# Performance work log

Measured on AMD Instinct MI355X. Metric: run time of the kernel, lower is better.

The kernel has to match this reference:

```python
import jax, jax.numpy as jnp
import numpy as np
import math

N, E, D, H, L, DIN, NEP = 20000, 320000, 128, 8, 4, 16, 4
DFF = 4 * D
DH = D // H
SCALE = 1.0 / math.sqrt(DH)


def _ln(x, s, b, eps=1e-5):
    mu = x.mean(-1, keepdims=True)
    var = ((x - mu) ** 2).mean(-1, keepdims=True)
    return (x - mu) * jax.lax.rsqrt(var + eps) * s + b


def _attn(h, src, dst, ew, Wq, Wk, Wv, Wo, Wo_b):
    n = h.shape[0]
    Q = (h @ Wq).reshape(n, H, DH)
    K = (h @ Wk).reshape(n, H, DH)
    V = (h @ Wv).reshape(n, H, DH)
    # per-edge scores: [E, H]; ew is sigmoid(edge_feat.sum(-1, keepdims)) -> [E, 1]
    scores = (Q[src] * K[dst]).sum(-1) * SCALE * ew
    msg = V[dst] * scores[:, :, None]                       # [E, H, DH]
    sums = jax.ops.segment_sum(msg, dst, num_segments=n)    # [N, H, DH]
    cnt = jax.ops.segment_sum(jnp.ones((msg.shape[0],), h.dtype), dst, num_segments=n)
    out = sums / jnp.maximum(cnt, 1.0)[:, None, None]       # segment-mean (zeros if no edges)
    return out.reshape(n, D) @ Wo + Wo_b


def setup_inputs() -> dict:
    key = jax.random.key(0)
    ks = iter(jax.random.split(key, 40))
    rn = lambda *s: jax.random.normal(next(ks), s, jnp.float32) * 0.02
    inp = {
        'x': jax.random.normal(next(ks), (N, DIN), jnp.float32),
        'edge_index': jax.random.randint(next(ks), (2, E), 0, N),
        'edge_attr': jax.random.normal(next(ks), (E, 1), jnp.float32),
        'in_w': rn(DIN, D), 'in_b': jnp.zeros((D,)),
        'ee_w1': rn(1, D // 4), 'ee_b1': jnp.zeros((D // 4,)),
        'ee_w2': rn(D // 4, D // 2), 'ee_b2': jnp.zeros((D // 2,)),
        'Wq': rn(L, D, D), 'Wk': rn(L, D, D), 'Wv': rn(L, D, D),
        'Wo': rn(L, D, D), 'Wo_b': jnp.zeros((L, D)),
        'ff_w1': rn(L, D, DFF), 'ff_b1': jnp.zeros((L, DFF)),
        'ff_w2': rn(L, DFF, D), 'ff_b2': jnp.zeros((L, D)),
        'ln1_s': jnp.ones((L, D)), 'ln1_b': jnp.zeros((L, D)),
        'ln2_s': jnp.ones((L, D)), 'ln2_b': jnp.zeros((L, D)),
        'ec_w1': rn(D * 2 + D // 2, D), 'ec_b1': jnp.zeros((D,)),
        'ec_w2': rn(D, D // 2), 'ec_b2': jnp.zeros((D // 2,)),
        'ec_w3': rn(D // 2, 1), 'ec_b3': jnp.zeros((1,)),
        'pp_w1': rn(D * 2 + D // 2, D), 'pp_b1': jnp.zeros((D,)),
        'pp_w2': rn(D, D // 2), 'pp_b2': jnp.zeros((D // 2,)),
        'pp_w3': rn(D // 2, NEP), 'pp_b3': jnp.zeros((NEP,)),
    }
    return inp


def reference(x, edge_index, edge_attr, in_w, in_b, ee_w1, ee_b1, ee_w2, ee_b2,
              Wq, Wk, Wv, Wo, Wo_b, ff_w1, ff_b1, ff_w2, ff_b2,
              ln1_s, ln1_b, ln2_s, ln2_b,
              ec_w1, ec_b1, ec_w2, ec_b2, ec_w3, ec_b3,
              pp_w1, pp_b1, pp_w2, pp_b2, pp_w3, pp_b3):
    src, dst = edge_index[0], edge_index[1]
    h = x @ in_w + in_b                                     # [N, D]
    edge_feat = jax.nn.relu(edge_attr @ ee_w1 + ee_b1) @ ee_w2 + ee_b2  # [E, D/2]
    ew = jax.nn.sigmoid(edge_feat.sum(-1, keepdims=True))   # [E, 1]
    for l in range(L):
        a = _attn(h, src, dst, ew, Wq[l], Wk[l], Wv[l], Wo[l], Wo_b[l])
        h = _ln(h + a, ln1_s[l], ln1_b[l])
        f = jax.nn.relu(h @ ff_w1[l] + ff_b1[l]) @ ff_w2[l] + ff_b2[l]
        h = _ln(h + f, ln2_s[l], ln2_b[l])
    ef = jnp.concatenate([h[src], h[dst], edge_feat], axis=1)  # [E, 2.5*D]
    z = jax.nn.relu(ef @ ec_w1 + ec_b1)
    z = jax.nn.relu(z @ ec_w2 + ec_b2)
    edge_logits = (z @ ec_w3 + ec_b3).squeeze(-1)
    p = jax.nn.relu(ef @ pp_w1 + pp_b1)
    p = jax.nn.relu(p @ pp_w2 + pp_b2)
    edge_params = jax.nn.softplus(p @ pp_w3 + pp_b3) + 1e-6
    return edge_logits, edge_params
```

## Files before the change

kernel.cpp:

```cpp
#include <hip/hip_runtime.h>
#include <hip/hip_bf16.h>
#include <math.h>

#define N_NODES 20000
#define N_EDGES 320000
#define D 128
#define DFF 512
#define DIN 16
#define NLAYER 4
#define SCALE 0.25f
#define KE1 288

typedef __hip_bfloat16 bf16;
typedef __attribute__((ext_vector_type(8))) __bf16 bf16x8_t;
typedef __attribute__((ext_vector_type(4))) float f32x4;

__global__ void k_input_proj(const float* __restrict__ x, const float* __restrict__ in_w,
                             const float* __restrict__ in_b, float* __restrict__ h,
                             __bf16* __restrict__ h_bf) {
  int node = blockIdx.x;
  int j = threadIdx.x;
  __shared__ float xs[DIN];
  if (j < DIN) xs[j] = x[node * DIN + j];
  __syncthreads();
  float acc = in_b[j];
  for (int k = 0; k < DIN; ++k) acc = fmaf(xs[k], in_w[k * D + j], acc);
  h[(size_t)node * D + j] = acc;
  h_bf[(size_t)node * D + j] = (__bf16)acc;
}

__global__ void k_edge_prep(const float* __restrict__ ea, const float* __restrict__ w1,
                            const float* __restrict__ b1, const float* __restrict__ w2,
                            const float* __restrict__ b2, const int* __restrict__ dst,
                            float* __restrict__ ew, float* __restrict__ cnt) {
  __shared__ float rs[32], w1s[32], b1s[32];
  __shared__ float b2sum;
  int tid = threadIdx.x;
  if (tid < 32) {
    float s = 0.f;
    for (int j = 0; j < 64; ++j) s += w2[tid * 64 + j];
    rs[tid] = s;
    w1s[tid] = w1[tid];
    b1s[tid] = b1[tid];
  }
  if (tid == 0) {
    float s = 0.f;
    for (int j = 0; j < 64; ++j) s += b2[j];
    b2sum = s;
  }
  __syncthreads();
  int e = blockIdx.x * blockDim.x + tid;
  if (e >= N_EDGES) return;
  float a = ea[e];
  float s = b2sum;
  for (int i = 0; i < 32; ++i) {
    float t = fmaxf(fmaf(a, w1s[i], b1s[i]), 0.f);
    s = fmaf(t, rs[i], s);
  }
  ew[e] = 1.f / (1.f + expf(-s));
  atomicAdd(&cnt[dst[e]], 1.f);
}

__global__ void k_cvt_all(const float* __restrict__ Wq, const float* __restrict__ Wk,
                          const float* __restrict__ Wv, const float* __restrict__ ffw1,
                          const float* __restrict__ ffw2, const float* __restrict__ Wo,
                          const float* __restrict__ ecw2, const float* __restrict__ ppw2,
                          __bf16* __restrict__ wqkvT, __bf16* __restrict__ w1T,
                          __bf16* __restrict__ w2T, __bf16* __restrict__ woT,
                          __bf16* __restrict__ w2ET, __bf16* __restrict__ w2PT) {
  int t = blockIdx.x * 256 + threadIdx.x;
  if (t < 196608) {
    int l = t / 49152, u = t % 49152;
    int m = u / 16384, v = u % 16384;
    int n = v / 128, k = v % 128;
    const float* W = (m == 0) ? Wq : (m == 1) ? Wk : Wv;
    wqkvT[t] = (__bf16)W[l * 16384 + k * 128 + n];
  } else if (t < 196608 + 262144) {
    int u = t - 196608;
    int l = u / 65536, v = u % 65536;
    int n = v / 128, k = v % 128;
    w1T[u] = (__bf16)ffw1[l * 65536 + k * 512 + n];
  } else if (t < 458752 + 262144) {
    int u = t - 458752;
    int l = u / 65536, v = u % 65536;
    int n = v / 512, k = v % 512;
    w2T[u] = (__bf16)ffw2[l * 65536 + k * 128 + n];
  } else if (t < 720896 + 65536) {
    int u = t - 720896;
    int l = u / 16384, v = u % 16384;
    int n = v / 128, k = v % 128;
    woT[u] = (__bf16)Wo[l * 16384 + k * 128 + n];
  } else if (t < 786432 + 8192) {
    int u = t - 786432;
    int n = u / 128, k = u % 128;
    w2ET[u] = (__bf16)ecw2[k * 64 + n];
  } else if (t < 794624 + 8192) {
    int u = t - 794624;
    int n = u / 128, k = u % 128;
    w2PT[u] = (__bf16)ppw2[k * 64 + n];
  }
}

__global__ void k_prep(const float* __restrict__ ec_w1, const float* __restrict__ ec_b1,
                       const float* __restrict__ pp_w1, const float* __restrict__ pp_b1,
                       const float* __restrict__ ee_w2, const float* __restrict__ ee_b2,
                       __bf16* __restrict__ w1ET, __bf16* __restrict__ w1PT,
                       float* __restrict__ b1Ep, float* __restrict__ b1Pp) {
  int tid = threadIdx.x;
  int p = tid >> 7, n = tid & 127;
  const float* w1 = p ? pp_w1 : ec_w1;
  const float* bb = p ? pp_b1 : ec_b1;
  __bf16* wT = p ? w1PT : w1ET;
  float* bo = p ? b1Pp : b1Ep;
  for (int k = 0; k < 256; ++k) wT[n * KE1 + k] = (__bf16)w1[k * 128 + n];
  for (int i = 0; i < 32; ++i) {
    float m = 0.f;
    for (int j = 0; j < 64; ++j) m = fmaf(ee_w2[i * 64 + j], w1[(256 + j) * 128 + n], m);
    wT[n * KE1 + 256 + i] = (__bf16)m;
  }
  float b = bb[n];
  for (int j = 0; j < 64; ++j) b = fmaf(ee_b2[j], w1[(256 + j) * 128 + n], b);
  bo[n] = b;
}

__global__ __launch_bounds__(256) void k_qkv(const __bf16* __restrict__ h_bf,
                                             const __bf16* __restrict__ wT,
                                             __bf16* __restrict__ Q, __bf16* __restrict__ K,
                                             __bf16* __restrict__ V) {
  int tid = threadIdx.x, wv = tid >> 6, lane = tid & 63;
  int lr = lane & 15, lk = (lane >> 4) * 8, g4 = (lane >> 4) * 4;
  int n0 = blockIdx.x * 16;
  const __bf16* hp = h_bf + (size_t)(n0 + lr) * D;
  f32x4 acc[6];
#pragma unroll
  for (int j = 0; j < 6; ++j) acc[j] = (f32x4){0.f, 0.f, 0.f, 0.f};
#pragma unroll
  for (int ks = 0; ks < 4; ++ks) {
    bf16x8_t aF = *(const bf16x8_t*)&hp[ks * 32 + lk];
#pragma unroll
    for (int j = 0; j < 6; ++j) {
      int nb = wv * 6 + j;
      bf16x8_t bF = *(const bf16x8_t*)&wT[(nb * 16 + lr) * 128 + ks * 32 + lk];
      acc[j] = __builtin_amdgcn_mfma_f32_16x16x32_bf16(aF, bF, acc[j], 0, 0, 0);
    }
  }
#pragma unroll
  for (int j = 0; j < 6; ++j) {
    int nb = wv * 6 + j;
    int m = nb >> 3;
    __bf16* out = (m == 0) ? Q : (m == 1) ? K : V;
#pragma unroll
    for (int r = 0; r < 4; ++r)
      out[(size_t)(n0 + g4 + r) * D + (nb & 7) * 16 + lr] = (__bf16)acc[j][r];
  }
}

__global__ void k_edge_attn(const int* __restrict__ src, const int* __restrict__ dst,
                            const float* __restrict__ ew, const __bf16* __restrict__ Q,
                            const __bf16* __restrict__ K, float* __restrict__ sc) {
  int t = blockIdx.x * blockDim.x + threadIdx.x;
  if (t >= N_EDGES * 8) return;
  int e = t >> 3, hd = t & 7;
  int s = src[e], d = dst[e];
  const __bf16* q = Q + (size_t)s * D + hd * 16;
  const __bf16* k = K + (size_t)d * D + hd * 16;
  bf16x8_t q0 = *(const bf16x8_t*)q, q1 = *(const bf16x8_t*)(q + 8);
  bf16x8_t k0 = *(const bf16x8_t*)k, k1 = *(const bf16x8_t*)(k + 8);
  float p = 0.f;
#pragma unroll
  for (int i = 0; i < 8; ++i) p = fmaf((float)q0[i], (float)k0[i], p);
#pragma unroll
  for (int i = 0; i < 8; ++i) p = fmaf((float)q1[i], (float)k1[i], p);
  atomicAdd(&sc[d * 8 + hd], p * SCALE * ew[e]);
}

__global__ __launch_bounds__(256) void k_node(
    float* __restrict__ sc, const float* __restrict__ cnt, const __bf16* __restrict__ Vin,
    float* __restrict__ h, __bf16* __restrict__ h_bf, const __bf16* __restrict__ woT,
    const float* __restrict__ Wo_b, const float* __restrict__ ln1_s,
    const float* __restrict__ ln1_b, const __bf16* __restrict__ w1T,
    const __bf16* __restrict__ w2T, const float* __restrict__ b1,
    const float* __restrict__ b2, const float* __restrict__ ln2_s,
    const float* __restrict__ ln2_b, const __bf16* __restrict__ wqkvT_next,
    __bf16* __restrict__ Q, __bf16* __restrict__ K, __bf16* __restrict__ Vout) {
  __shared__ __bf16 z0[16][136];
  __shared__ __bf16 z1[16][520];
  __shared__ float lnb[4][16][2];
  int tid = threadIdx.x, wv = tid >> 6, lane = tid & 63;
  int lr = lane & 15, lk = (lane >> 4) * 8, g4 = (lane >> 4) * 4;
  int n0 = blockIdx.x * 16;
  int nd = n0 + lr;

  float inv = 1.f / fmaxf(cnt[nd], 1.f);
  float scs[8];
#pragma unroll
  for (int i = 0; i < 8; ++i) scs[i] = sc[nd * 8 + i] * inv;
  f32x4 acc[2];
#pragma unroll
  for (int j = 0; j < 2; ++j) {
    float bv = Wo_b[(wv * 2 + j) * 16 + lr];
    acc[j] = (f32x4){bv, bv, bv, bv};
  }
#pragma unroll
  for (int ks = 0; ks < 4; ++ks) {
    bf16x8_t v8 = *(const bf16x8_t*)&Vin[(size_t)nd * D + ks * 32 + lk];
    float m = scs[(ks * 32 + lk) >> 4];
    bf16x8_t aF;
#pragma unroll
    for (int i = 0; i < 8; ++i) aF[i] = (__bf16)((float)v8[i] * m);
#pragma unroll
    for (int j = 0; j < 2; ++j) {
      bf16x8_t bF = *(const bf16x8_t*)&woT[((wv * 2 + j) * 16 + lr) * 128 + ks * 32 + lk];
      acc[j] = __builtin_amdgcn_mfma_f32_16x16x32_bf16(aF, bF, acc[j], 0, 0, 0);
    }
  }
  float y[2][4];
#pragma unroll
  for (int j = 0; j < 2; ++j)
#pragma unroll
    for (int r = 0; r < 4; ++r)
      y[j][r] = h[(size_t)(n0 + g4 + r) * D + (wv * 2 + j) * 16 + lr] + acc[j][r];
  float s_[4], q_[4];
#pragma unroll
  for (int r = 0; r < 4; ++r) {
    float a0 = y[0][r], a1 = y[1][r];
    float s = a0 + a1, q = fmaf(a0, a0, a1 * a1);
    s += __shfl_xor(s, 1); s += __shfl_xor(s, 2); s += __shfl_xor(s, 4); s += __shfl_xor(s, 8);
    q += __shfl_xor(q, 1); q += __shfl_xor(q, 2); q += __shfl_xor(q, 4); q += __shfl_xor(q, 8);
    s_[r] = s; q_[r] = q;
  }
  if (lr == 0) {
#pragma unroll
    for (int r = 0; r < 4; ++r) {
      lnb[wv][g4 + r][0] = s_[r];
      lnb[wv][g4 + r][1] = q_[r];
    }
  }
  __syncthreads();
  if (tid < 128) sc[n0 * 8 + tid] = 0.f;
  float mean[4], rstd[4];
#pragma unroll
  for (int r = 0; r < 4; ++r) {
    float sm = 0.f, sq = 0.f;
#pragma unroll
    for (int w2i = 0; w2i < 4; ++w2i) {
      sm += lnb[w2i][g4 + r][0];
      sq += lnb[w2i][g4 + r][1];
    }
    float mu = sm * (1.f / 128.f);
    mean[r] = mu;
    rstd[r] = rsqrtf(sq * (1.f / 128.f) - mu * mu + 1e-5f);
  }
#pragma unroll
  for (int j = 0; j < 2; ++j) {
    int col = (wv * 2 + j) * 16 + lr;
    float lsv = ln1_s[col], lbv = ln1_b[col];
#pragma unroll
    for (int r = 0; r < 4; ++r) {
      y[j][r] = (y[j][r] - mean[r]) * rstd[r] * lsv + lbv;
      z0[g4 + r][col] = (__bf16)y[j][r];
    }
  }
  __syncthreads();

  f32x4 a1[8];
#pragma unroll
  for (int j = 0; j < 8; ++j) {
    float bv = b1[(wv * 8 + j) * 16 + lr];
    a1[j] = (f32x4){bv, bv, bv, bv};
  }
#pragma unroll
  for (int ks = 0; ks < 4; ++ks) {
    bf16x8_t aF = *(const bf16x8_t*)&z0[lr][ks * 32 + lk];
#pragma unroll
    for (int j = 0; j < 8; ++j) {
      bf16x8_t bF = *(const bf16x8_t*)&w1T[((wv * 8 + j) * 16 + lr) * 128 + ks * 32 + lk];
      a1[j] = __builtin_amdgcn_mfma_f32_16x16x32_bf16(aF, bF, a1[j], 0, 0, 0);
    }
  }
#pragma unroll
  for (int j = 0; j < 8; ++j)
#pragma unroll
    for (int r = 0; r < 4; ++r)
      z1[g4 + r][(wv * 8 + j) * 16 + lr] = (__bf16)fmaxf(a1[j][r], 0.f);
  __syncthreads();

  f32x4 a2[2];
#pragma unroll
  for (int j = 0; j < 2; ++j) {
    float bv = b2[(wv * 2 + j) * 16 + lr];
    a2[j] = (f32x4){bv, bv, bv, bv};
  }
#pragma unroll
  for (int ks = 0; ks < 16; ++ks) {
    bf16x8_t aF = *(const bf16x8_t*)&z1[lr][ks * 32 + lk];
#pragma unroll
    for (int j = 0; j < 2; ++j) {
      bf16x8_t bF = *(const bf16x8_t*)&w2T[((wv * 2 + j) * 16 + lr) * 512 + ks * 32 + lk];
      a2[j] = __builtin_amdgcn_mfma_f32_16x16x32_bf16(aF, bF, a2[j], 0, 0, 0);
    }
  }
#pragma unroll
  for (int j = 0; j < 2; ++j)
#pragma unroll
    for (int r = 0; r < 4; ++r) y[j][r] += a2[j][r];
#pragma unroll
  for (int r = 0; r < 4; ++r) {
    float a0 = y[0][r], a1v = y[1][r];
    float s = a0 + a1v, q = fmaf(a0, a0, a1v * a1v);
    s += __shfl_xor(s, 1); s += __shfl_xor(s, 2); s += __shfl_xor(s, 4); s += __shfl_xor(s, 8);
    q += __shfl_xor(q, 1); q += __shfl_xor(q, 2); q += __shfl_xor(q, 4); q += __shfl_xor(q, 8);
    s_[r] = s; q_[r] = q;
  }
  if (lr == 0) {
#pragma unroll
    for (int r = 0; r < 4; ++r) {
      lnb[wv][g4 + r][0] = s_[r];
      lnb[wv][g4 + r][1] = q_[r];
    }
  }
  __syncthreads();
#pragma unroll
  for (int r = 0; r < 4; ++r) {
    float sm = 0.f, sq = 0.f;
#pragma unroll
    for (int w2i = 0; w2i < 4; ++w2i) {
      sm += lnb[w2i][g4 + r][0];
      sq += lnb[w2i][g4 + r][1];
    }
    float mu = sm * (1.f / 128.f);
    mean[r] = mu;
    rstd[r] = rsqrtf(sq * (1.f / 128.f) - mu * mu + 1e-5f);
  }
#pragma unroll
  for (int j = 0; j < 2; ++j) {
    int col = (wv * 2 + j) * 16 + lr;
    float lsv = ln2_s[col], lbv = ln2_b[col];
#pragma unroll
    for (int r = 0; r < 4; ++r) {
      float yv = (y[j][r] - mean[r]) * rstd[r] * lsv + lbv;
      y[j][r] = yv;
      h[(size_t)(n0 + g4 + r) * D + col] = yv;
      h_bf[(size_t)(n0 + g4 + r) * D + col] = (__bf16)yv;
    }
  }

  if (wqkvT_next) {
#pragma unroll
    for (int j = 0; j < 2; ++j)
#pragma unroll
      for (int r = 0; r < 4; ++r)
        z0[g4 + r][(wv * 2 + j) * 16 + lr] = (__bf16)y[j][r];
    __syncthreads();
    f32x4 aq[6];
#pragma unroll
    for (int j = 0; j < 6; ++j) aq[j] = (f32x4){0.f, 0.f, 0.f, 0.f};
#pragma unroll
    for (int ks = 0; ks < 4; ++ks) {
      bf16x8_t aF = *(const bf16x8_t*)&z0[lr][ks * 32 + lk];
#pragma unroll
      for (int j = 0; j < 6; ++j) {
        int nb = wv * 6 + j;
        bf16x8_t bF = *(const bf16x8_t*)&wqkvT_next[(nb * 16 + lr) * 128 + ks * 32 + lk];
        aq[j] = __builtin_amdgcn_mfma_f32_16x16x32_bf16(aF, bF, aq[j], 0, 0, 0);
      }
    }
#pragma unroll
    for (int j = 0; j < 6; ++j) {
      int nb = wv * 6 + j;
      int m = nb >> 3;
      __bf16* out = (m == 0) ? Q : (m == 1) ? K : Vout;
#pragma unroll
      for (int r = 0; r < 4; ++r)
        out[(size_t)(n0 + g4 + r) * D + (nb & 7) * 16 + lr] = (__bf16)aq[j][r];
    }
  }
}

__global__ __launch_bounds__(256) void k_pnode(const __bf16* __restrict__ h_bf,
                                               const __bf16* __restrict__ w1ET,
                                               const __bf16* __restrict__ w1PT,
                                               __bf16* __restrict__ PsE,
                                               __bf16* __restrict__ PdE,
                                               __bf16* __restrict__ PsP,
                                               __bf16* __restrict__ PdP) {
  int tid = threadIdx.x, wv = tid >> 6, lane = tid & 63;
  int lr = lane & 15, lk = (lane >> 4) * 8, g4 = (lane >> 4) * 4;
  int n0 = blockIdx.x * 16;
  const __bf16* hp = h_bf + (size_t)(n0 + lr) * D;
  const __bf16* wsrc = (wv & 2) ? w1PT : w1ET;
  int koff = (wv & 1) ? 128 : 0;
  __bf16* out = (wv == 0) ? PsE : (wv == 1) ? PdE : (wv == 2) ? PsP : PdP;
  f32x4 acc[8];
#pragma unroll
  for (int nb = 0; nb < 8; ++nb) acc[nb] = (f32x4){0.f, 0.f, 0.f, 0.f};
#pragma unroll
  for (int ks = 0; ks < 4; ++ks) {
    bf16x8_t aF = *(const bf16x8_t*)&hp[ks * 32 + lk];
#pragma unroll
    for (int nb = 0; nb < 8; ++nb) {
      bf16x8_t bF = *(const bf16x8_t*)&wsrc[(nb * 16 + lr) * KE1 + koff + ks * 32 + lk];
      acc[nb] = __builtin_amdgcn_mfma_f32_16x16x32_bf16(aF, bF, acc[nb], 0, 0, 0);
    }
  }
#pragma unroll
  for (int nb = 0; nb < 8; ++nb)
#pragma unroll
    for (int r = 0; r < 4; ++r)
      out[(size_t)(n0 + g4 + r) * D + nb * 16 + lr] = (__bf16)acc[nb][r];
}

__global__ __launch_bounds__(256) void k_final(
    const int* __restrict__ src, const int* __restrict__ dst, const float* __restrict__ ea,
    const float* __restrict__ ee_w1, const float* __restrict__ ee_b1,
    const __bf16* __restrict__ w1ET, const __bf16* __restrict__ w1PT,
    const __bf16* __restrict__ w2ET, const __bf16* __restrict__ w2PT,
    const float* __restrict__ b1Ep, const float* __restrict__ b1Pp,
    const __bf16* __restrict__ PsE, const __bf16* __restrict__ PdE,
    const __bf16* __restrict__ PsP, const __bf16* __restrict__ PdP,
    const float* __restrict__ ec_b2, const float* __restrict__ ec_w3,
    const float* __restrict__ ec_b3, const float* __restrict__ pp_b2,
    const float* __restrict__ pp_w3, const float* __restrict__ pp_b3,
    float* __restrict__ out_logits, float* __restrict__ out_params) {
  __shared__ __bf16 z1[2][32][136];
  __shared__ __bf16 zf[4][16][136];
  int tid = threadIdx.x, wv = tid >> 6, lane = tid & 63;
  int lr = lane & 15, lk = (lane >> 4) * 8, g4 = (lane >> 4) * 4;
  int p = wv & 1, m0 = (wv >> 1) * 16;
  int e0 = blockIdx.x * 32;
  int e = e0 + m0 + lr;
  float av = ea[e];
  bf16x8_t aR;
#pragma unroll
  for (int i = 0; i < 8; ++i)
    aR[i] = (__bf16)fmaxf(fmaf(av, ee_w1[lk + i], ee_b1[lk + i]), 0.f);

  const __bf16* w1x = p ? w1PT : w1ET;
  const float* b1x = p ? b1Pp : b1Ep;
  const __bf16* w2x = p ? w2PT : w2ET;
  const float* b2x = p ? pp_b2 : ec_b2;

  f32x4 acc[8];
#pragma unroll
  for (int nb = 0; nb < 8; ++nb) {
    float bv = b1x[nb * 16 + lr];
    acc[nb] = (f32x4){bv, bv, bv, bv};
  }
#pragma unroll
  for (int nb = 0; nb < 8; ++nb) {
    bf16x8_t bF = *(const bf16x8_t*)&w1x[(nb * 16 + lr) * KE1 + 256 + lk];
    acc[nb] = __builtin_amdgcn_mfma_f32_16x16x32_bf16(aR, bF, acc[nb], 0, 0, 0);
  }
#pragma unroll
  for (int nb = 0; nb < 8; ++nb)
#pragma unroll
    for (int r = 0; r < 4; ++r) zf[wv][g4 + r][nb * 16 + lr] = (__bf16)acc[nb][r];

  {
    int em = lane >> 2, c4 = lane & 3;
    int ee = e0 + m0 + em;
    const __bf16* Ps = p ? PsP : PsE;
    const __bf16* Pd = p ? PdP : PdE;
    const __bf16* psrow = Ps + (size_t)src[ee] * D + c4 * 32;
    const __bf16* pdrow = Pd + (size_t)dst[ee] * D + c4 * 32;
#pragma unroll
    for (int ch = 0; ch < 4; ++ch) {
      bf16x8_t a = *(const bf16x8_t*)&psrow[ch * 8];
      bf16x8_t b = *(const bf16x8_t*)&pdrow[ch * 8];
      bf16x8_t f = *(const bf16x8_t*)&zf[wv][em][c4 * 32 + ch * 8];
      bf16x8_t o;
#pragma unroll
      for (int i = 0; i < 8; ++i)
        o[i] = (__bf16)fmaxf((float)a[i] + (float)b[i] + (float)f[i], 0.f);
      *(bf16x8_t*)&z1[p][m0 + em][c4 * 32 + ch * 8] = o;
    }
  }

  f32x4 acc2[4];
#pragma unroll
  for (int nb = 0; nb < 4; ++nb) {
    float bv = b2x[nb * 16 + lr];
    acc2[nb] = (f32x4){bv, bv, bv, bv};
  }
#pragma unroll
  for (int ks = 0; ks < 4; ++ks) {
    bf16x8_t aF = *(const bf16x8_t*)&z1[p][m0 + lr][ks * 32 + lk];
#pragma unroll
    for (int nb = 0; nb < 4; ++nb) {
      bf16x8_t bF = *(const bf16x8_t*)&w2x[(nb * 16 + lr) * 128 + ks * 32 + lk];
      acc2[nb] = __builtin_amdgcn_mfma_f32_16x16x32_bf16(aF, bF, acc2[nb], 0, 0, 0);
    }
  }

  if (p == 0) {
    float w3v[4];
#pragma unroll
    for (int nb = 0; nb < 4; ++nb) w3v[nb] = ec_w3[nb * 16 + lr];
    float b3 = ec_b3[0];
#pragma unroll
    for (int r = 0; r < 4; ++r) {
      float s = 0.f;
#pragma unroll
      for (int nb = 0; nb < 4; ++nb) s = fmaf(fmaxf(acc2[nb][r], 0.f), w3v[nb], s);
      s += __shfl_xor(s, 1);
      s += __shfl_xor(s, 2);
      s += __shfl_xor(s, 4);
      s += __shfl_xor(s, 8);
      if (lr == 0) out_logits[e0 + m0 + g4 + r] = s + b3;
    }
  } else {
    float wp[4][4];
#pragma unroll
    for (int nb = 0; nb < 4; ++nb)
#pragma unroll
      for (int c = 0; c < 4; ++c) wp[nb][c] = pp_w3[(nb * 16 + lr) * 4 + c];
#pragma unroll
    for (int c = 0; c < 4; ++c) {
      float b3 = pp_b3[c];
#pragma unroll
      for (int r = 0; r < 4; ++r) {
        float s = 0.f;
#pragma unroll
        for (int nb = 0; nb < 4; ++nb) s = fmaf(fmaxf(acc2[nb][r], 0.f), wp[nb][c], s);
        s += __shfl_xor(s, 1);
        s += __shfl_xor(s, 2);
        s += __shfl_xor(s, 4);
        s += __shfl_xor(s, 8);
        if (lr == 0) {
          float xx = s + b3;
          float sp = fmaxf(xx, 0.f) + log1pf(expf(-fabsf(xx)));
          out_params[(size_t)(e0 + m0 + g4 + r) * 4 + c] = sp + 1e-6f;
        }
      }
    }
  }
}

extern "C" void kernel_launch(void* const* d_in, const int* in_sizes, int n_in,
                              void* d_out, int out_size, void* d_ws, size_t ws_size,
                              hipStream_t stream) {
  const float* x = (const float*)d_in[0];
  const int* eidx = (const int*)d_in[1];
  const float* eattr = (const float*)d_in[2];
  const float* in_w = (const float*)d_in[3];
  const float* in_b = (const float*)d_in[4];
  const float* ee_w1 = (const float*)d_in[5];
  const float* ee_b1 = (const float*)d_in[6];
  const float* ee_w2 = (const float*)d_in[7];
  const float* ee_b2 = (const float*)d_in[8];
  const float* Wq = (const float*)d_in[9];
  const float* Wk = (const float*)d_in[10];
  const float* Wv = (const float*)d_in[11];
  const float* Wo = (const float*)d_in[12];
  const float* Wo_b = (const float*)d_in[13];
  const float* ff_w1 = (const float*)d_in[14];
  const float* ff_b1 = (const float*)d_in[15];
  const float* ff_w2 = (const float*)d_in[16];
  const float* ff_b2 = (const float*)d_in[17];
  const float* ln1_s = (const float*)d_in[18];
  const float* ln1_b = (const float*)d_in[19];
  const float* ln2_s = (const float*)d_in[20];
  const float* ln2_b = (const float*)d_in[21];
  const float* ec_w1 = (const float*)d_in[22];
  const float* ec_b1 = (const float*)d_in[23];
  const float* ec_w2 = (const float*)d_in[24];
  const float* ec_b2 = (const float*)d_in[25];
  const float* ec_w3 = (const float*)d_in[26];
  const float* ec_b3 = (const float*)d_in[27];
  const float* pp_w1 = (const float*)d_in[28];
  const float* pp_b1 = (const float*)d_in[29];
  const float* pp_w2 = (const float*)d_in[30];
  const float* pp_b2 = (const float*)d_in[31];
  const float* pp_w3 = (const float*)d_in[32];
  const float* pp_b3 = (const float*)d_in[33];

  const int* src = eidx;
  const int* dst = eidx + N_EDGES;

  char* wsb = (char*)d_ws;
  float* sc = (float*)wsb;
  float* cnt = (float*)(wsb + 640000);
  float* h = (float*)(wsb + 720000);
  __bf16* h_bf = (__bf16*)(wsb + 10960000);
  __bf16* Q = (__bf16*)(wsb + 16080000);
  __bf16* Kb = (__bf16*)(wsb + 21200000);
  __bf16* V0 = (__bf16*)(wsb + 26320000);
  __bf16* V1 = (__bf16*)(wsb + 31440000);
  float* ew = (float*)(wsb + 36560000);
  __bf16* wqkvT = (__bf16*)(wsb + 37840000);
  __bf16* w1T = (__bf16*)(wsb + 38233216);
  __bf16* w2T = (__bf16*)(wsb + 38757504);
  __bf16* woT = (__bf16*)(wsb + 39281792);
  __bf16* w1ET = (__bf16*)(wsb + 39412864);
  __bf16* w1PT = (__bf16*)(wsb + 39486592);
  __bf16* w2ET = (__bf16*)(wsb + 39560320);
  __bf16* w2PT = (__bf16*)(wsb + 39576704);
  float* b1Ep = (float*)(wsb + 39593088);
  float* b1Pp = (float*)(wsb + 39593600);

  hipMemsetAsync(cnt, 0, N_NODES * sizeof(float), stream);
  hipMemsetAsync(sc, 0, N_NODES * 8 * sizeof(float), stream);
  k_input_proj<<<N_NODES, D, 0, stream>>>(x, in_w, in_b, h, h_bf);
  k_edge_prep<<<(N_EDGES + 255) / 256, 256, 0, stream>>>(eattr, ee_w1, ee_b1, ee_w2, ee_b2,
                                                         dst, ew, cnt);
  k_cvt_all<<<(802816 + 255) / 256, 256, 0, stream>>>(Wq, Wk, Wv, ff_w1, ff_w2, Wo, ec_w2,
                                                      pp_w2, wqkvT, w1T, w2T, woT, w2ET, w2PT);
  k_prep<<<1, 256, 0, stream>>>(ec_w1, ec_b1, pp_w1, pp_b1, ee_w2, ee_b2, w1ET, w1PT, b1Ep,
                                b1Pp);

  int nblk = N_NODES / 16;
  k_qkv<<<nblk, 256, 0, stream>>>(h_bf, wqkvT, Q, Kb, V0);
  for (int l = 0; l < NLAYER; ++l) {
    __bf16* Vin = (l & 1) ? V1 : V0;
    __bf16* Vout = (l & 1) ? V0 : V1;
    k_edge_attn<<<(N_EDGES * 8 + 255) / 256, 256, 0, stream>>>(src, dst, ew, Q, Kb, sc);
    k_node<<<nblk, 256, 0, stream>>>(
        sc, cnt, Vin, h, h_bf, woT + (size_t)l * 16384, Wo_b + l * D, ln1_s + l * D,
        ln1_b + l * D, w1T + (size_t)l * 65536, w2T + (size_t)l * 65536, ff_b1 + l * DFF,
        ff_b2 + l * D, ln2_s + l * D, ln2_b + l * D,
        (l < NLAYER - 1) ? (wqkvT + (size_t)(l + 1) * 49152) : (const __bf16*)nullptr, Q, Kb,
        Vout);
  }

  __bf16* PsE = Q;
  __bf16* PdE = Kb;
  __bf16* PsP = V0;
  __bf16* PdP = V1;
  k_pnode<<<nblk, 256, 0, stream>>>(h_bf, w1ET, w1PT, PsE, PdE, PsP, PdP);

  float* out_logits = (float*)d_out;
  float* out_params = out_logits + N_EDGES;
  k_final<<<N_EDGES / 32, 256, 0, stream>>>(src, dst, eattr, ee_w1, ee_b1, w1ET, w1PT, w2ET,
                                            w2PT, b1Ep, b1Pp, PsE, PdE, PsP, PdP, ec_b2,
                                            ec_w3, ec_b3, pp_b2, pp_w3, pp_b3, out_logits,
                                            out_params);
}
```

Baseline: 615.3 us.

## Replace atomic edge attention with dst-sorted CSR gather and fuse edge-node projection

Builds a destination-sorted CSR once, using a single-block prefix scan over counts and then an atomic-cursor scatter of src and edge weight. Per-layer attention then runs one wave per destination node. Each wave first accumulates the weighted sum of the gathered Q rows and takes one dot product with K[d], using linearity. This removes the per-edge, per-head float atomics and the per-layer memset of scores. The separate k_pnode projection is folded into the last layer's k_node, which reuses the LayerNorm output already held in shared memory. The cost is a serial one-block scan, an extra scatter pass, and an edge order inside each CSR segment that is not deterministic.

```diff
diff --git a/kernel.cpp b/kernel.cpp
--- a/kernel.cpp
+++ b/kernel.cpp
@@ -13,6 +13,7 @@
 
 typedef __hip_bfloat16 bf16;
 typedef __attribute__((ext_vector_type(8))) __bf16 bf16x8_t;
+typedef __attribute__((ext_vector_type(2))) __bf16 bf16x2_t;
 typedef __attribute__((ext_vector_type(4))) float f32x4;
 
 __global__ void k_input_proj(const float* __restrict__ x, const float* __restrict__ in_w,
@@ -59,6 +60,48 @@
   }
   ew[e] = 1.f / (1.f + expf(-s));
   atomicAdd(&cnt[dst[e]], 1.f);
+}
+
+__global__ __launch_bounds__(1024) void k_scan(const float* __restrict__ cnt,
+                                               int* __restrict__ off,
+                                               int* __restrict__ cursor) {
+  __shared__ int ts[1024];
+  int tid = threadIdx.x;
+  const int per = (N_NODES + 1023) / 1024;
+  int base = tid * per;
+  int s = 0;
+  for (int i = 0; i < per; ++i) {
+    int idx = base + i;
+    if (idx < N_NODES) s += (int)cnt[idx];
+  }
+  ts[tid] = s;
+  __syncthreads();
+  for (int st = 1; st < 1024; st <<= 1) {
+    int v = (tid >= st) ? ts[tid - st] : 0;
+    __syncthreads();
+    ts[tid] += v;
+    __syncthreads();
+  }
+  int run = (tid == 0) ? 0 : ts[tid - 1];
+  for (int i = 0; i < per; ++i) {
+    int idx = base + i;
+    if (idx < N_NODES) {
+      off[idx] = run;
+      cursor[idx] = run;
+      run += (int)cnt[idx];
+    }
+  }
+  if (tid == 1023) off[N_NODES] = run;
+}
+
+__global__ void k_scatter(const int* __restrict__ src, const int* __restrict__ dst,
+                          const float* __restrict__ ew, int* __restrict__ cursor,
+                          int* __restrict__ csr_src, float* __restrict__ csr_ew) {
+  int e = blockIdx.x * blockDim.x + threadIdx.x;
+  if (e >= N_EDGES) return;
+  int pos = atomicAdd(&cursor[dst[e]], 1);
+  csr_src[pos] = src[e];
+  csr_ew[pos] = ew[e];
 }
 
 __global__ void k_cvt_all(const float* __restrict__ Wq, const float* __restrict__ Wk,
@@ -155,34 +198,54 @@
   }
 }
 
-__global__ void k_edge_attn(const int* __restrict__ src, const int* __restrict__ dst,
-                            const float* __restrict__ ew, const __bf16* __restrict__ Q,
-                            const __bf16* __restrict__ K, float* __restrict__ sc) {
-  int t = blockIdx.x * blockDim.x + threadIdx.x;
-  if (t >= N_EDGES * 8) return;
-  int e = t >> 3, hd = t & 7;
-  int s = src[e], d = dst[e];
-  const __bf16* q = Q + (size_t)s * D + hd * 16;
-  const __bf16* k = K + (size_t)d * D + hd * 16;
-  bf16x8_t q0 = *(const bf16x8_t*)q, q1 = *(const bf16x8_t*)(q + 8);
-  bf16x8_t k0 = *(const bf16x8_t*)k, k1 = *(const bf16x8_t*)(k + 8);
-  float p = 0.f;
-#pragma unroll
-  for (int i = 0; i < 8; ++i) p = fmaf((float)q0[i], (float)k0[i], p);
-#pragma unroll
-  for (int i = 0; i < 8; ++i) p = fmaf((float)q1[i], (float)k1[i], p);
-  atomicAdd(&sc[d * 8 + hd], p * SCALE * ew[e]);
+__global__ __launch_bounds__(256) void k_attn_csr(const int* __restrict__ off,
+                                                  const int* __restrict__ csr_src,
+                                                  const float* __restrict__ csr_ew,
+                                                  const __bf16* __restrict__ Q,
+                                                  const __bf16* __restrict__ K,
+                                                  float* __restrict__ sc) {
+  int wv = threadIdx.x >> 6, lane = threadIdx.x & 63;
+  int d = blockIdx.x * 4 + wv;
+  bf16x2_t k2 = *(const bf16x2_t*)(K + (size_t)d * D + lane * 2);
+  float t0 = 0.f, t1 = 0.f;
+  int i = off[d], end = off[d + 1];
+  int s_next = 0;
+  float w_next = 0.f;
+  if (i < end) {
+    s_next = csr_src[i];
+    w_next = csr_ew[i];
+  }
+  while (i < end) {
+    int s = s_next;
+    float w = w_next;
+    ++i;
+    if (i < end) {
+      s_next = csr_src[i];
+      w_next = csr_ew[i];
+    }
+    bf16x2_t q2 = *(const bf16x2_t*)(Q + (size_t)s * D + lane * 2);
+    t0 = fmaf(w, (float)q2[0], t0);
+    t1 = fmaf(w, (float)q2[1], t1);
+  }
+  float p = fmaf(t0, (float)k2[0], t1 * (float)k2[1]);
+  p += __shfl_xor(p, 1);
+  p += __shfl_xor(p, 2);
+  p += __shfl_xor(p, 4);
+  if ((lane & 7) == 0) sc[d * 8 + (lane >> 3)] = p * SCALE;
 }
 
 __global__ __launch_bounds__(256) void k_node(
-    float* __restrict__ sc, const float* __restrict__ cnt, const __bf16* __restrict__ Vin,
-    float* __restrict__ h, __bf16* __restrict__ h_bf, const __bf16* __restrict__ woT,
-    const float* __restrict__ Wo_b, const float* __restrict__ ln1_s,
-    const float* __restrict__ ln1_b, const __bf16* __restrict__ w1T,
-    const __bf16* __restrict__ w2T, const float* __restrict__ b1,
-    const float* __restrict__ b2, const float* __restrict__ ln2_s,
-    const float* __restrict__ ln2_b, const __bf16* __restrict__ wqkvT_next,
-    __bf16* __restrict__ Q, __bf16* __restrict__ K, __bf16* __restrict__ Vout) {
+    const float* __restrict__ sc, const float* __restrict__ cnt,
+    const __bf16* __restrict__ Vin, float* __restrict__ h, __bf16* __restrict__ h_bf,
+    const __bf16* __restrict__ woT, const float* __restrict__ Wo_b,
+    const float* __restrict__ ln1_s, const float* __restrict__ ln1_b,
+    const __bf16* __restrict__ w1T, const __bf16* __restrict__ w2T,
+    const float* __restrict__ b1, const float* __restrict__ b2,
+    const float* __restrict__ ln2_s, const float* __restrict__ ln2_b,
+    const __bf16* __restrict__ wqkvT_next, __bf16* __restrict__ Q, __bf16* __restrict__ K,
+    __bf16* __restrict__ Vout, const __bf16* __restrict__ w1ET,
+    const __bf16* __restrict__ w1PT, __bf16* __restrict__ PsE, __bf16* __restrict__ PdE,
+    __bf16* __restrict__ PsP, __bf16* __restrict__ PdP) {
   __shared__ __bf16 z0[16][136];
   __shared__ __bf16 z1[16][520];
   __shared__ float lnb[4][16][2];
@@ -237,7 +300,6 @@
     }
   }
   __syncthreads();
-  if (tid < 128) sc[n0 * 8 + tid] = 0.f;
   float mean[4], rstd[4];
 #pragma unroll
   for (int r = 0; r < 4; ++r) {
@@ -345,13 +407,14 @@
     }
   }
 
+#pragma unroll
+  for (int j = 0; j < 2; ++j)
+#pragma unroll
+    for (int r = 0; r < 4; ++r)
+      z0[g4 + r][(wv * 2 + j) * 16 + lr] = (__bf16)y[j][r];
+  __syncthreads();
+
   if (wqkvT_next) {
-#pragma unroll
-    for (int j = 0; j < 2; ++j)
-#pragma unroll
-      for (int r = 0; r < 4; ++r)
-        z0[g4 + r][(wv * 2 + j) * 16 + lr] = (__bf16)y[j][r];
-    __syncthreads();
     f32x4 aq[6];
 #pragma unroll
     for (int j = 0; j < 6; ++j) aq[j] = (f32x4){0.f, 0.f, 0.f, 0.f};
@@ -374,40 +437,28 @@
       for (int r = 0; r < 4; ++r)
         out[(size_t)(n0 + g4 + r) * D + (nb & 7) * 16 + lr] = (__bf16)aq[j][r];
     }
-  }
-}
-
-__global__ __launch_bounds__(256) void k_pnode(const __bf16* __restrict__ h_bf,
-                                               const __bf16* __restrict__ w1ET,
-                                               const __bf16* __restrict__ w1PT,
-                                               __bf16* __restrict__ PsE,
-                                               __bf16* __restrict__ PdE,
-                                               __bf16* __restrict__ PsP,
-                                               __bf16* __restrict__ PdP) {
-  int tid = threadIdx.x, wv = tid >> 6, lane = tid & 63;
-  int lr = lane & 15, lk = (lane >> 4) * 8, g4 = (lane >> 4) * 4;
-  int n0 = blockIdx.x * 16;
-  const __bf16* hp = h_bf + (size_t)(n0 + lr) * D;
-  const __bf16* wsrc = (wv & 2) ? w1PT : w1ET;
-  int koff = (wv & 1) ? 128 : 0;
-  __bf16* out = (wv == 0) ? PsE : (wv == 1) ? PdE : (wv == 2) ? PsP : PdP;
-  f32x4 acc[8];
-#pragma unroll
-  for (int nb = 0; nb < 8; ++nb) acc[nb] = (f32x4){0.f, 0.f, 0.f, 0.f};
-#pragma unroll
-  for (int ks = 0; ks < 4; ++ks) {
-    bf16x8_t aF = *(const bf16x8_t*)&hp[ks * 32 + lk];
-#pragma unroll
-    for (int nb = 0; nb < 8; ++nb) {
-      bf16x8_t bF = *(const bf16x8_t*)&wsrc[(nb * 16 + lr) * KE1 + koff + ks * 32 + lk];
-      acc[nb] = __builtin_amdgcn_mfma_f32_16x16x32_bf16(aF, bF, acc[nb], 0, 0, 0);
-    }
-  }
-#pragma unroll
-  for (int nb = 0; nb < 8; ++nb)
-#pragma unroll
-    for (int r = 0; r < 4; ++r)
-      out[(size_t)(n0 + g4 + r) * D + nb * 16 + lr] = (__bf16)acc[nb][r];
+  } else {
+    const __bf16* wsrc = (wv & 2) ? w1PT : w1ET;
+    int koff = (wv & 1) ? 128 : 0;
+    __bf16* outP = (wv == 0) ? PsE : (wv == 1) ? PdE : (wv == 2) ? PsP : PdP;
+    f32x4 ap[8];
+#pragma unroll
+    for (int nb = 0; nb < 8; ++nb) ap[nb] = (f32x4){0.f, 0.f, 0.f, 0.f};
+#pragma unroll
+    for (int ks = 0; ks < 4; ++ks) {
+      bf16x8_t aF = *(const bf16x8_t*)&z0[lr][ks * 32 + lk];
+#pragma unroll
+      for (int nb = 0; nb < 8; ++nb) {
+        bf16x8_t bF = *(const bf16x8_t*)&wsrc[(nb * 16 + lr) * KE1 + koff + ks * 32 + lk];
+        ap[nb] = __builtin_amdgcn_mfma_f32_16x16x32_bf16(aF, bF, ap[nb], 0, 0, 0);
+      }
+    }
+#pragma unroll
+    for (int nb = 0; nb < 8; ++nb)
+#pragma unroll
+      for (int r = 0; r < 4; ++r)
+        outP[(size_t)(n0 + g4 + r) * D + nb * 16 + lr] = (__bf16)ap[nb][r];
+  }
 }
 
 __global__ __launch_bounds__(256) void k_final(
@@ -597,36 +648,40 @@
   __bf16* w2PT = (__bf16*)(wsb + 39576704);
   float* b1Ep = (float*)(wsb + 39593088);
   float* b1Pp = (float*)(wsb + 39593600);
+  int* off = (int*)(wsb + 39594112);
+  int* cursor = (int*)(wsb + 39674128);
+  int* csr_src = (int*)(wsb + 39754128);
+  float* csr_ew = (float*)(wsb + 41034128);
 
   hipMemsetAsync(cnt, 0, N_NODES * sizeof(float), stream);
-  hipMemsetAsync(sc, 0, N_NODES * 8 * sizeof(float), stream);
   k_input_proj<<<N_NODES, D, 0, stream>>>(x, in_w, in_b, h, h_bf);
   k_edge_prep<<<(N_EDGES + 255) / 256, 256, 0, stream>>>(eattr, ee_w1, ee_b1, ee_w2, ee_b2,
                                                          dst, ew, cnt);
+  k_scan<<<1, 1024, 0, stream>>>(cnt, off, cursor);
+  k_scatter<<<(N_EDGES + 255) / 256, 256, 0, stream>>>(src, dst, ew, cursor, csr_src, csr_ew);
   k_cvt_all<<<(802816 + 255) / 256, 256, 0, stream>>>(Wq, Wk, Wv, ff_w1, ff_w2, Wo, ec_w2,
                                                       pp_w2, wqkvT, w1T, w2T, woT, w2ET, w2PT);
   k_prep<<<1, 256, 0, stream>>>(ec_w1, ec_b1, pp_w1, pp_b1, ee_w2, ee_b2, w1ET, w1PT, b1Ep,
                                 b1Pp);
+
+  __bf16* PsE = Q;
+  __bf16* PdE = Kb;
+  __bf16* PsP = V0;
+  __bf16* PdP = V1;
 
   int nblk = N_NODES / 16;
   k_qkv<<<nblk, 256, 0, stream>>>(h_bf, wqkvT, Q, Kb, V0);
   for (int l = 0; l < NLAYER; ++l) {
     __bf16* Vin = (l & 1) ? V1 : V0;
     __bf16* Vout = (l & 1) ? V0 : V1;
-    k_edge_attn<<<(N_EDGES * 8 + 255) / 256, 256, 0, stream>>>(src, dst, ew, Q, Kb, sc);
+    k_attn_csr<<<N_NODES / 4, 256, 0, stream>>>(off, csr_src, csr_ew, Q, Kb, sc);
     k_node<<<nblk, 256, 0, stream>>>(
         sc, cnt, Vin, h, h_bf, woT + (size_t)l * 16384, Wo_b + l * D, ln1_s + l * D,
         ln1_b + l * D, w1T + (size_t)l * 65536, w2T + (size_t)l * 65536, ff_b1 + l * DFF,
         ff_b2 + l * D, ln2_s + l * D, ln2_b + l * D,
         (l < NLAYER - 1) ? (wqkvT + (size_t)(l + 1) * 49152) : (const __bf16*)nullptr, Q, Kb,
-        Vout);
-  }
-
-  __bf16* PsE = Q;
-  __bf16* PdE = Kb;
-  __bf16* PsP = V0;
-  __bf16* PdP = V1;
-  k_pnode<<<nblk, 256, 0, stream>>>(h_bf, w1ET, w1PT, PsE, PdE, PsP, PdP);
+        Vout, w1ET, w1PT, PsE, PdE, PsP, PdP);
+  }
 
   float* out_logits = (float*)d_out;
   float* out_params = out_logits + N_EDGES;
```

Result: slower. 678.0 us (+10.2%).

## Sort edges by destination for final edge MLP and fuse pnode projection into last layer

Applied to the files above, without the earlier changes.

Builds a destination-sorted edge order (counting-sort scan plus atomic scatter) and has the final edge kernel walk edges in that order, gathering PdE/PdP rows with locality and scattering outputs back by original edge id. It also folds the separate per-node edge-head projection kernel into the last k_node launch, reusing the LN output already staged in shared memory. This removes one launch and one re-read of h_bf, and improves cache reuse on dst gathers. It adds a single-block scan, an atomic scatter pass and indirect output writes.

```diff
diff --git a/kernel.cpp b/kernel.cpp
--- a/kernel.cpp
+++ b/kernel.cpp
@@ -59,6 +59,50 @@
   }
   ew[e] = 1.f / (1.f + expf(-s));
   atomicAdd(&cnt[dst[e]], 1.f);
+}
+
+__global__ __launch_bounds__(1024) void k_scan(const float* __restrict__ cnt,
+                                               int* __restrict__ off,
+                                               int* __restrict__ cursor) {
+  __shared__ int ts[1024];
+  int tid = threadIdx.x;
+  const int per = (N_NODES + 1023) / 1024;
+  int base = tid * per;
+  int s = 0;
+  for (int i = 0; i < per; ++i) {
+    int idx = base + i;
+    if (idx < N_NODES) s += (int)cnt[idx];
+  }
+  ts[tid] = s;
+  __syncthreads();
+  for (int st = 1; st < 1024; st <<= 1) {
+    int v = (tid >= st) ? ts[tid - st] : 0;
+    __syncthreads();
+    ts[tid] += v;
+    __syncthreads();
+  }
+  int run = (tid == 0) ? 0 : ts[tid - 1];
+  for (int i = 0; i < per; ++i) {
+    int idx = base + i;
+    if (idx < N_NODES) {
+      off[idx] = run;
+      cursor[idx] = run;
+      run += (int)cnt[idx];
+    }
+  }
+  if (tid == 1023) off[N_NODES] = run;
+}
+
+__global__ void k_scatter(const int* __restrict__ src, const int* __restrict__ dst,
+                          int* __restrict__ cursor, int* __restrict__ csr_src,
+                          int* __restrict__ csr_dst, int* __restrict__ csr_eid) {
+  int e = blockIdx.x * blockDim.x + threadIdx.x;
+  if (e >= N_EDGES) return;
+  int d = dst[e];
+  int pos = atomicAdd(&cursor[d], 1);
+  csr_src[pos] = src[e];
+  csr_dst[pos] = d;
+  csr_eid[pos] = e;
 }
 
 __global__ void k_cvt_all(const float* __restrict__ Wq, const float* __restrict__ Wk,
@@ -182,7 +226,10 @@
     const __bf16* __restrict__ w2T, const float* __restrict__ b1,
     const float* __restrict__ b2, const float* __restrict__ ln2_s,
     const float* __restrict__ ln2_b, const __bf16* __restrict__ wqkvT_next,
-    __bf16* __restrict__ Q, __bf16* __restrict__ K, __bf16* __restrict__ Vout) {
+    __bf16* __restrict__ Q, __bf16* __restrict__ K, __bf16* __restrict__ Vout,
+    const __bf16* __restrict__ w1ET, const __bf16* __restrict__ w1PT,
+    __bf16* __restrict__ PsE, __bf16* __restrict__ PdE, __bf16* __restrict__ PsP,
+    __bf16* __restrict__ PdP) {
   __shared__ __bf16 z0[16][136];
   __shared__ __bf16 z1[16][520];
   __shared__ float lnb[4][16][2];
@@ -345,13 +392,14 @@
     }
   }
 
+#pragma unroll
+  for (int j = 0; j < 2; ++j)
+#pragma unroll
+    for (int r = 0; r < 4; ++r)
+      z0[g4 + r][(wv * 2 + j) * 16 + lr] = (__bf16)y[j][r];
+  __syncthreads();
+
   if (wqkvT_next) {
-#pragma unroll
-    for (int j = 0; j < 2; ++j)
-#pragma unroll
-      for (int r = 0; r < 4; ++r)
-        z0[g4 + r][(wv * 2 + j) * 16 + lr] = (__bf16)y[j][r];
-    __syncthreads();
     f32x4 aq[6];
 #pragma unroll
     for (int j = 0; j < 6; ++j) aq[j] = (f32x4){0.f, 0.f, 0.f, 0.f};
@@ -374,44 +422,33 @@
       for (int r = 0; r < 4; ++r)
         out[(size_t)(n0 + g4 + r) * D + (nb & 7) * 16 + lr] = (__bf16)aq[j][r];
     }
-  }
-}
-
-__global__ __launch_bounds__(256) void k_pnode(const __bf16* __restrict__ h_bf,
-                                               const __bf16* __restrict__ w1ET,
-                                               const __bf16* __restrict__ w1PT,
-                                               __bf16* __restrict__ PsE,
-                                               __bf16* __restrict__ PdE,
-                                               __bf16* __restrict__ PsP,
-                                               __bf16* __restrict__ PdP) {
-  int tid = threadIdx.x, wv = tid >> 6, lane = tid & 63;
-  int lr = lane & 15, lk = (lane >> 4) * 8, g4 = (lane >> 4) * 4;
-  int n0 = blockIdx.x * 16;
-  const __bf16* hp = h_bf + (size_t)(n0 + lr) * D;
-  const __bf16* wsrc = (wv & 2) ? w1PT : w1ET;
-  int koff = (wv & 1) ? 128 : 0;
-  __bf16* out = (wv == 0) ? PsE : (wv == 1) ? PdE : (wv == 2) ? PsP : PdP;
-  f32x4 acc[8];
-#pragma unroll
-  for (int nb = 0; nb < 8; ++nb) acc[nb] = (f32x4){0.f, 0.f, 0.f, 0.f};
-#pragma unroll
-  for (int ks = 0; ks < 4; ++ks) {
-    bf16x8_t aF = *(const bf16x8_t*)&hp[ks * 32 + lk];
-#pragma unroll
-    for (int nb = 0; nb < 8; ++nb) {
-      bf16x8_t bF = *(const bf16x8_t*)&wsrc[(nb * 16 + lr) * KE1 + koff + ks * 32 + lk];
-      acc[nb] = __builtin_amdgcn_mfma_f32_16x16x32_bf16(aF, bF, acc[nb], 0, 0, 0);
-    }
-  }
-#pragma unroll
-  for (int nb = 0; nb < 8; ++nb)
-#pragma unroll
-    for (int r = 0; r < 4; ++r)
-      out[(size_t)(n0 + g4 + r) * D + nb * 16 + lr] = (__bf16)acc[nb][r];
+  } else {
+    const __bf16* wsrc = (wv & 2) ? w1PT : w1ET;
+    int koff = (wv & 1) ? 128 : 0;
+    __bf16* outP = (wv == 0) ? PsE : (wv == 1) ? PdE : (wv == 2) ? PsP : PdP;
+    f32x4 ap[8];
+#pragma unroll
+    for (int nb = 0; nb < 8; ++nb) ap[nb] = (f32x4){0.f, 0.f, 0.f, 0.f};
+#pragma unroll
+    for (int ks = 0; ks < 4; ++ks) {
+      bf16x8_t aF = *(const bf16x8_t*)&z0[lr][ks * 32 + lk];
+#pragma unroll
+      for (int nb = 0; nb < 8; ++nb) {
+        bf16x8_t bF = *(const bf16x8_t*)&wsrc[(nb * 16 + lr) * KE1 + koff + ks * 32 + lk];
+        ap[nb] = __builtin_amdgcn_mfma_f32_16x16x32_bf16(aF, bF, ap[nb], 0, 0, 0);
+      }
+    }
+#pragma unroll
+    for (int nb = 0; nb < 8; ++nb)
+#pragma unroll
+      for (int r = 0; r < 4; ++r)
+        outP[(size_t)(n0 + g4 + r) * D + nb * 16 + lr] = (__bf16)ap[nb][r];
+  }
 }
 
 __global__ __launch_bounds__(256) void k_final(
-    const int* __restrict__ src, const int* __restrict__ dst, const float* __restrict__ ea,
+    const int* __restrict__ csr_src, const int* __restrict__ csr_dst,
+    const int* __restrict__ csr_eid, const float* __restrict__ ea,
     const float* __restrict__ ee_w1, const float* __restrict__ ee_b1,
     const __bf16* __restrict__ w1ET, const __bf16* __restrict__ w1PT,
     const __bf16* __restrict__ w2ET, const __bf16* __restrict__ w2PT,
@@ -429,7 +466,8 @@
   int p = wv & 1, m0 = (wv >> 1) * 16;
   int e0 = blockIdx.x * 32;
   int e = e0 + m0 + lr;
-  float av = ea[e];
+  int eid = csr_eid[e];
+  float av = ea[eid];
   bf16x8_t aR;
 #pragma unroll
   for (int i = 0; i < 8; ++i)
@@ -461,8 +499,8 @@
     int ee = e0 + m0 + em;
     const __bf16* Ps = p ? PsP : PsE;
     const __bf16* Pd = p ? PdP : PdE;
-    const __bf16* psrow = Ps + (size_t)src[ee] * D + c4 * 32;
-    const __bf16* pdrow = Pd + (size_t)dst[ee] * D + c4 * 32;
+    const __bf16* psrow = Ps + (size_t)csr_src[ee] * D + c4 * 32;
+    const __bf16* pdrow = Pd + (size_t)csr_dst[ee] * D + c4 * 32;
 #pragma unroll
     for (int ch = 0; ch < 4; ++ch) {
       bf16x8_t a = *(const bf16x8_t*)&psrow[ch * 8];
@@ -506,7 +544,7 @@
       s += __shfl_xor(s, 2);
       s += __shfl_xor(s, 4);
       s += __shfl_xor(s, 8);
-      if (lr == 0) out_logits[e0 + m0 + g4 + r] = s + b3;
+      if (lr == 0) out_logits[csr_eid[e0 + m0 + g4 + r]] = s + b3;
     }
   } else {
     float wp[4][4];
@@ -529,7 +567,7 @@
         if (lr == 0) {
           float xx = s + b3;
           float sp = fmaxf(xx, 0.f) + log1pf(expf(-fabsf(xx)));
-          out_params[(size_t)(e0 + m0 + g4 + r) * 4 + c] = sp + 1e-6f;
+          out_params[(size_t)csr_eid[e0 + m0 + g4 + r] * 4 + c] = sp + 1e-6f;
         }
       }
     }
@@ -597,16 +635,29 @@
   __bf16* w2PT = (__bf16*)(wsb + 39576704);
   float* b1Ep = (float*)(wsb + 39593088);
   float* b1Pp = (float*)(wsb + 39593600);
+  int* off = (int*)(wsb + 39594112);
+  int* cursor = (int*)(wsb + 39674128);
+  int* csr_src = (int*)(wsb + 39754128);
+  int* csr_dst = (int*)(wsb + 41034128);
+  int* csr_eid = (int*)(wsb + 42314128);
 
   hipMemsetAsync(cnt, 0, N_NODES * sizeof(float), stream);
   hipMemsetAsync(sc, 0, N_NODES * 8 * sizeof(float), stream);
   k_input_proj<<<N_NODES, D, 0, stream>>>(x, in_w, in_b, h, h_bf);
   k_edge_prep<<<(N_EDGES + 255) / 256, 256, 0, stream>>>(eattr, ee_w1, ee_b1, ee_w2, ee_b2,
                                                          dst, ew, cnt);
+  k_scan<<<1, 1024, 0, stream>>>(cnt, off, cursor);
+  k_scatter<<<(N_EDGES + 255) / 256, 256, 0, stream>>>(src, dst, cursor, csr_src, csr_dst,
+                                                       csr_eid);
   k_cvt_all<<<(802816 + 255) / 256, 256, 0, stream>>>(Wq, Wk, Wv, ff_w1, ff_w2, Wo, ec_w2,
                                                       pp_w2, wqkvT, w1T, w2T, woT, w2ET, w2PT);
   k_prep<<<1, 256, 0, stream>>>(ec_w1, ec_b1, pp_w1, pp_b1, ee_w2, ee_b2, w1ET, w1PT, b1Ep,
                                 b1Pp);
+
+  __bf16* PsE = Q;
+  __bf16* PdE = Kb;
+  __bf16* PsP = V0;
+  __bf16* PdP = V1;
 
   int nblk = N_NODES / 16;
   k_qkv<<<nblk, 256, 0, stream>>>(h_bf, wqkvT, Q, Kb, V0);
@@ -619,19 +670,13 @@
         ln1_b + l * D, w1T + (size_t)l * 65536, w2T + (size_t)l * 65536, ff_b1 + l * DFF,
         ff_b2 + l * D, ln2_s + l * D, ln2_b + l * D,
         (l < NLAYER - 1) ? (wqkvT + (size_t)(l + 1) * 49152) : (const __bf16*)nullptr, Q, Kb,
-        Vout);
-  }
-
-  __bf16* PsE = Q;
-  __bf16* PdE = Kb;
-  __bf16* PsP = V0;
-  __bf16* PdP = V1;
-  k_pnode<<<nblk, 256, 0, stream>>>(h_bf, w1ET, w1PT, PsE, PdE, PsP, PdP);
+        Vout, w1ET, w1PT, PsE, PdE, PsP, PdP);
+  }
 
   float* out_logits = (float*)d_out;
   float* out_params = out_logits + N_EDGES;
-  k_final<<<N_EDGES / 32, 256, 0, stream>>>(src, dst, eattr, ee_w1, ee_b1, w1ET, w1PT, w2ET,
-                                            w2PT, b1Ep, b1Pp, PsE, PdE, PsP, PdP, ec_b2,
-                                            ec_w3, ec_b3, pp_b2, pp_w3, pp_b3, out_logits,
-                                            out_params);
-}
+  k_final<<<N_EDGES / 32, 256, 0, stream>>>(csr_src, csr_dst, csr_eid, eattr, ee_w1, ee_b1,
+                                            w1ET, w1PT, w2ET, w2PT, b1Ep, b1Pp, PsE, PdE,
+                                            PsP, PdP, ec_b2, ec_w3, ec_b3, pp_b2, pp_w3,
+                                            pp_b3, out_logits, out_params);
+}
```

Result: slower. 698.2 us (+13.5%).
